# Kernel tuning notes

Measured on AMD Instinct MI355X. Metric: run time of the kernel, lower is better.

## Reference

```python
import jax, jax.numpy as jnp
import numpy as np

NUM_HEADS = 12
SPARSITY = 0.5

def setup_inputs() -> dict:
    key = jax.random.key(0)
    ks = jax.random.split(key, 5)
    B, N, C = 16, 577, 768
    x = jax.random.normal(ks[0], (B, N, C), dtype=jnp.float32)
    x_original = jax.random.normal(ks[1], (B, N, C), dtype=jnp.float32)
    qkv_w = jax.random.normal(ks[2], (3 * C, C), dtype=jnp.float32) * (C ** -0.5)
    proj_w = jax.random.normal(ks[3], (C, C), dtype=jnp.float32) * (C ** -0.5)
    proj_b = jax.random.normal(ks[4], (C,), dtype=jnp.float32) * 0.01
    return {"x": x, "x_original": x_original, "qkv_w": qkv_w,
            "proj_w": proj_w, "proj_b": proj_b, "num_prop": 57}

def reference(x, x_original, qkv_w, proj_w, proj_b, num_prop):
    B, N, C = x.shape
    H = NUM_HEADS
    hd = C // H
    scale = hd ** -0.5
    # qkv projection (no bias): [B,N,3C] -> q,k,v each [B,H,N,hd]
    qkv = (x @ qkv_w.T).reshape(B, N, 3, H, hd).transpose(2, 0, 3, 1, 4)
    q, k, v = qkv[0], qkv[1], qkv[2]
    attn = jax.nn.softmax(jnp.einsum('bhnd,bhmd->bhnm', q * scale, k), axis=-1)
    # sparsity threshold: keep entries >= the int(N*N*sparsity)-th largest per (b,h)
    if SPARSITY < 1:
        flat = attn.reshape(B, H, N * N)
        desc = -jnp.sort(-flat, axis=-1)  # descending
        sigma = desc[:, :, int(N * N * SPARSITY)][:, :, None, None]
        attn = jnp.where(attn >= sigma, attn, jnp.zeros((), attn.dtype))
    if num_prop > 0:
        K = N - num_prop  # tokens kept (incl. CLS)
        # token importance: max over heads of attention diagonal (excluding CLS)
        diag = jnp.diagonal(attn, axis1=-2, axis2=-1)[:, :, 1:]  # [B,H,N-1]
        token_rank = jnp.argsort(-diag.max(axis=1), axis=1)      # [B,N-1] desc
        index_kept = token_rank[:, :N - 1 - num_prop] + 1        # [B,K-1]
        index_kept = jnp.concatenate(
            [jnp.zeros((B, 1), index_kept.dtype), index_kept], axis=1)  # [B,K]
        # gather kept query rows of attn: [B,H,K,N]
        idx = jnp.broadcast_to(index_kept[:, None, :, None], (B, H, K, N))
        attn_kept = jnp.take_along_axis(attn, idx, axis=2)
        x_original = jnp.take_along_axis(
            x_original, jnp.broadcast_to(index_kept[:, :, None], (B, K, C)), axis=1)
        out = jnp.einsum('bhkn,bhnd->bhkd', attn_kept, v)
        out = out.transpose(0, 2, 1, 3).reshape(B, K, C)
    else:
        out = jnp.einsum('bhnm,bhmd->bhnd', attn, v)
        out = out.transpose(0, 2, 1, 3).reshape(B, N, C)
    out = out @ proj_w.T + proj_b
    return (out, x_original)
```

## Files before the change

### kernel.cpp

```cpp
#include <hip/hip_runtime.h>
#include <cstdint>
#include <cstddef>


namespace {
constexpr int B_  = 16;
constexpr int N_  = 577;
constexpr int C_  = 768;
constexpr int H_  = 12;
constexpr int HD_ = 64;
constexpr int BH_ = B_ * H_;
constexpr int KK_ = N_ - 57;
constexpr unsigned KIDX_ = 166464u;
constexpr int M1_ = B_ * N_;
constexpr int M2_ = B_ * KK_;
}

__device__ __forceinline__ void fma4(const float4& a, const float4& b, float& acc) {
  acc = __builtin_fmaf(a.x, b.x, acc);
  acc = __builtin_fmaf(a.y, b.y, acc);
  acc = __builtin_fmaf(a.z, b.z, acc);
  acc = __builtin_fmaf(a.w, b.w, acc);
}

__global__ __launch_bounds__(256) void qkv_gemm(
    const float* __restrict__ X, const float* __restrict__ W,
    float* __restrict__ qb, float* __restrict__ kb, float* __restrict__ vb) {
  __shared__ __align__(16) float Xs[64][68];
  __shared__ __align__(16) float Ws2[128][68];
  const int m0 = blockIdx.x * 64;
  const int n0 = blockIdx.y * 128;
  const int t = threadIdx.x;
  const int tx = t & 15, ty = t >> 4;
  float acc[4][8] = {};
  for (int k0 = 0; k0 < 768; k0 += 64) {
    __syncthreads();
    {
      const int c = t & 15, r0 = t >> 4;
#pragma unroll
      for (int s = 0; s < 4; s++) {
        int r = r0 + 16 * s;
        int gm = m0 + r;
        float4 v = make_float4(0.f, 0.f, 0.f, 0.f);
        if (gm < M1_) v = *(const float4*)&X[(size_t)gm * 768 + k0 + 4 * c];
        *(float4*)&Xs[r][4 * c] = v;
      }
#pragma unroll
      for (int s = 0; s < 8; s++) {
        int r = r0 + 16 * s;
        float4 v = *(const float4*)&W[(size_t)(n0 + r) * 768 + k0 + 4 * c];
        *(float4*)&Ws2[r][4 * c] = v;
      }
    }
    __syncthreads();
#pragma unroll 2
    for (int d4 = 0; d4 < 16; d4++) {
      float4 a4[4], b4[8];
#pragma unroll
      for (int i = 0; i < 4; i++) a4[i] = *(const float4*)&Xs[tx + 16 * i][4 * d4];
#pragma unroll
      for (int j = 0; j < 8; j++) b4[j] = *(const float4*)&Ws2[ty + 16 * j][4 * d4];
#pragma unroll
      for (int i = 0; i < 4; i++)
#pragma unroll
        for (int j = 0; j < 8; j++) fma4(a4[i], b4[j], acc[i][j]);
    }
  }
  for (int i = 0; i < 4; i++) {
    int gm = m0 + tx + 16 * i;
    if (gm >= M1_) continue;
    int b = gm / N_, n = gm % N_;
    for (int j = 0; j < 8; j++) {
      int gn = n0 + ty + 16 * j;
      int which = gn / C_, rem = gn % C_;
      int h = rem >> 6, d = rem & 63;
      float* dst = (which == 0) ? qb : (which == 1) ? kb : vb;
      dst[(((size_t)(b * H_ + h)) * N_ + n) * HD_ + d] = acc[i][j];
    }
  }
}

__global__ __launch_bounds__(256) void attn_stats(
    const float* __restrict__ qb, const float* __restrict__ kb,
    float* __restrict__ rowmax_g, float* __restrict__ rowsum_g,
    float* __restrict__ ldiag) {
  __shared__ __align__(16) float Qs[64][68];
  __shared__ __align__(16) float Ksf[128][68];
  const int bh = blockIdx.x;
  const int q0 = blockIdx.y * 64;
  const int t = threadIdx.x;
  const int tx = t & 15, ty = t >> 4;
  {
    const int c = t & 15, r0 = t >> 4;
#pragma unroll
    for (int s = 0; s < 4; s++) {
      int r = r0 + 16 * s;
      int gq = q0 + r;
      float4 v = make_float4(0.f, 0.f, 0.f, 0.f);
      if (gq < N_) v = *(const float4*)&qb[((size_t)bh * N_ + gq) * HD_ + 4 * c];
      v.x *= 0.125f; v.y *= 0.125f; v.z *= 0.125f; v.w *= 0.125f;
      *(float4*)&Qs[r][4 * c] = v;
    }
  }
  float m[4], ss[4];
#pragma unroll
  for (int i = 0; i < 4; i++) { m[i] = -INFINITY; ss[i] = 0.f; }
  for (int n0 = 0; n0 < N_; n0 += 128) {
    __syncthreads();
    {
      const int c = t & 15, r0 = t >> 4;
#pragma unroll
      for (int s = 0; s < 8; s++) {
        int r = r0 + 16 * s;
        int gn = n0 + r;
        float4 v = make_float4(0.f, 0.f, 0.f, 0.f);
        if (gn < N_) v = *(const float4*)&kb[((size_t)bh * N_ + gn) * HD_ + 4 * c];
        *(float4*)&Ksf[r][4 * c] = v;
      }
    }
    __syncthreads();
    float l[4][8];
#pragma unroll
    for (int i = 0; i < 4; i++)
#pragma unroll
      for (int j = 0; j < 8; j++) l[i][j] = 0.f;
#pragma unroll 2
    for (int d4 = 0; d4 < 16; d4++) {
      float4 a4[4], b4[8];
#pragma unroll
      for (int i = 0; i < 4; i++) a4[i] = *(const float4*)&Qs[tx + 16 * i][4 * d4];
#pragma unroll
      for (int j = 0; j < 8; j++) b4[j] = *(const float4*)&Ksf[ty + 16 * j][4 * d4];
#pragma unroll
      for (int i = 0; i < 4; i++)
#pragma unroll
        for (int j = 0; j < 8; j++) fma4(a4[i], b4[j], l[i][j]);
    }
#pragma unroll
    for (int i = 0; i < 4; i++) {
      int gq = q0 + tx + 16 * i;
      float tmax = -INFINITY;
#pragma unroll
      for (int j = 0; j < 8; j++)
        if (n0 + ty + 16 * j < N_) tmax = fmaxf(tmax, l[i][j]);
      float mn = fmaxf(m[i], tmax);
      ss[i] *= expf(m[i] - mn);
#pragma unroll
      for (int j = 0; j < 8; j++) {
        int col = n0 + ty + 16 * j;
        if (col < N_) {
          ss[i] += expf(l[i][j] - mn);
          if (col == gq) ldiag[(size_t)bh * N_ + gq] = l[i][j];
        }
      }
      m[i] = mn;
    }
  }
  __syncthreads();
  float* Mred = &Ksf[0][0];
  float* Sred = &Ksf[0][0] + 1024;
#pragma unroll
  for (int i = 0; i < 4; i++) {
    int row = tx + 16 * i;
    Mred[row * 16 + ty] = m[i];
    Sred[row * 16 + ty] = ss[i];
  }
  __syncthreads();
  if (t < 64) {
    int gq = q0 + t;
    if (gq < N_) {
      float M = -INFINITY;
      for (int k = 0; k < 16; k++) M = fmaxf(M, Mred[t * 16 + k]);
      float S = 0.f;
      for (int k = 0; k < 16; k++) S += expf(Mred[t * 16 + k] - M) * Sred[t * 16 + k];
      rowmax_g[(size_t)bh * N_ + gq] = M;
      rowsum_g[(size_t)bh * N_ + gq] = S;
    }
  }
}

template <int MODE>
__global__ __launch_bounds__(256) void hist_pass(
    const float* __restrict__ qb, const float* __restrict__ kb,
    const float* __restrict__ rowmax_g, const float* __restrict__ rowsum_g,
    const unsigned* __restrict__ pfx_in, unsigned* __restrict__ hist_out) {
  constexpr int HB = (MODE == 2) ? 256 : 4096;
  __shared__ __align__(16) float Qs[64][68];
  __shared__ __align__(16) float Ksf[128][68];
  __shared__ unsigned hloc[HB];
  const int bh = blockIdx.x;
  const int q0 = blockIdx.y * 64;
  const int t = threadIdx.x;
  const int tx = t & 15, ty = t >> 4;
  for (int i = t; i < HB; i += 256) hloc[i] = 0u;
  const unsigned pf = (MODE == 0) ? 0u : pfx_in[bh];
  {
    const int c = t & 15, r0 = t >> 4;
#pragma unroll
    for (int s = 0; s < 4; s++) {
      int r = r0 + 16 * s;
      int gq = q0 + r;
      float4 v = make_float4(0.f, 0.f, 0.f, 0.f);
      if (gq < N_) v = *(const float4*)&qb[((size_t)bh * N_ + gq) * HD_ + 4 * c];
      v.x *= 0.125f; v.y *= 0.125f; v.z *= 0.125f; v.w *= 0.125f;
      *(float4*)&Qs[r][4 * c] = v;
    }
  }
  float M[4], inv[4];
#pragma unroll
  for (int i = 0; i < 4; i++) {
    int gq = q0 + tx + 16 * i;
    if (gq < N_) {
      M[i] = rowmax_g[(size_t)bh * N_ + gq];
      inv[i] = 1.f / rowsum_g[(size_t)bh * N_ + gq];
    } else { M[i] = 0.f; inv[i] = 0.f; }
  }
  for (int n0 = 0; n0 < N_; n0 += 128) {
    __syncthreads();
    {
      const int c = t & 15, r0 = t >> 4;
#pragma unroll
      for (int s = 0; s < 8; s++) {
        int r = r0 + 16 * s;
        int gn = n0 + r;
        float4 v = make_float4(0.f, 0.f, 0.f, 0.f);
        if (gn < N_) v = *(const float4*)&kb[((size_t)bh * N_ + gn) * HD_ + 4 * c];
        *(float4*)&Ksf[r][4 * c] = v;
      }
    }
    __syncthreads();
    float l[4][8];
#pragma unroll
    for (int i = 0; i < 4; i++)
#pragma unroll
      for (int j = 0; j < 8; j++) l[i][j] = 0.f;
#pragma unroll 2
    for (int d4 = 0; d4 < 16; d4++) {
      float4 a4[4], b4[8];
#pragma unroll
      for (int i = 0; i < 4; i++) a4[i] = *(const float4*)&Qs[tx + 16 * i][4 * d4];
#pragma unroll
      for (int j = 0; j < 8; j++) b4[j] = *(const float4*)&Ksf[ty + 16 * j][4 * d4];
#pragma unroll
      for (int i = 0; i < 4; i++)
#pragma unroll
        for (int j = 0; j < 8; j++) fma4(a4[i], b4[j], l[i][j]);
    }
#pragma unroll
    for (int i = 0; i < 4; i++) {
      int gq = q0 + tx + 16 * i;
#pragma unroll
      for (int j = 0; j < 8; j++) {
        bool valid = (gq < N_) && (n0 + ty + 16 * j < N_);
        if (MODE == 0) {
          unsigned bin = 0xFFFFu;
          if (valid) {
            float e = expf(l[i][j] - M[i]);
            float v = e * inv[i];
            bin = __float_as_uint(v) >> 20;
          }
          unsigned lead = (unsigned)__builtin_amdgcn_readfirstlane((int)bin);
          unsigned long long mm = __ballot(bin == lead);
          if (bin == lead) {
            if (lead != 0xFFFFu && (t & 63) == (__ffsll((unsigned long long)mm) - 1))
              atomicAdd(&hloc[lead], (unsigned)__popcll(mm));
          } else if (bin != 0xFFFFu) {
            atomicAdd(&hloc[bin], 1u);
          }
        } else if (valid) {
          float e = expf(l[i][j] - M[i]);
          float v = e * inv[i];
          unsigned bits = __float_as_uint(v);
          if (MODE == 1) {
            if ((bits >> 20) == pf) atomicAdd(&hloc[(bits >> 8) & 0xFFFu], 1u);
          } else {
            if ((bits >> 8) == pf) atomicAdd(&hloc[bits & 0xFFu], 1u);
          }
        }
      }
    }
  }
  __syncthreads();
  for (int i = t; i < HB; i += 256)
    if (hloc[i]) atomicAdd(&hist_out[(size_t)bh * HB + i], hloc[i]);
}

__global__ __launch_bounds__(64) void select_level(
    const unsigned* __restrict__ hist, int nbins,
    const unsigned* __restrict__ krem_in, const unsigned* __restrict__ pfx_in,
    unsigned* __restrict__ krem_out, unsigned* __restrict__ pfx_out, int shift) {
  const int bh = blockIdx.x;
  const int l = threadIdx.x;
  const int seg = nbins / 64;
  const unsigned krem = krem_in ? krem_in[bh] : KIDX_;
  const unsigned* hb = hist + (size_t)bh * nbins;
  __shared__ unsigned ps[64];
  unsigned psum = 0;
  int hi = nbins - 1 - l * seg;
  for (int i = 0; i < seg; i++) psum += hb[hi - i];
  ps[l] = psum;
  __syncthreads();
  if (l == 0) {
    unsigned cum = 0, before = 0;
    int bin = 0;
    for (int j = 0; j < 64; j++) {
      if (cum + ps[j] > krem) {
        unsigned c = cum;
        int hj = nbins - 1 - j * seg;
        for (int i = 0; i < seg; i++) {
          unsigned cnt = hb[hj - i];
          if (c + cnt > krem) { bin = hj - i; before = c; break; }
          c += cnt;
        }
        break;
      }
      cum += ps[j];
    }
    unsigned p = pfx_in ? pfx_in[bh] : 0u;
    pfx_out[bh] = (p << shift) | (unsigned)bin;
    krem_out[bh] = krem - before;
  }
}

__global__ __launch_bounds__(576) void rank_kernel(
    const float* __restrict__ ldiag, const float* __restrict__ rowmax_g,
    const float* __restrict__ rowsum_g, const unsigned* __restrict__ sigbits,
    int* __restrict__ kept) {
  const int b = blockIdx.x;
  const int i = threadIdx.x;
  __shared__ float sc[576];
  float s = 0.f;
  for (int h = 0; h < H_; h++) {
    int bh = b * H_ + h;
    float l = ldiag[(size_t)bh * N_ + (i + 1)];
    float M = rowmax_g[(size_t)bh * N_ + (i + 1)];
    float inv = 1.f / rowsum_g[(size_t)bh * N_ + (i + 1)];
    float e = expf(l - M);
    float v = e * inv;
    float sg = __uint_as_float(sigbits[bh]);
    if (v >= sg) s = fmaxf(s, v);
  }
  sc[i] = s;
  __syncthreads();
  int r = 0;
  for (int j = 0; j < 576; j++) {
    float sj = sc[j];
    if (sj > s || (sj == s && j < i)) r++;
  }
  if (r < KK_ - 1) kept[b * KK_ + r + 1] = i + 1;
  if (i == 0) kept[b * KK_] = 0;
}

__global__ __launch_bounds__(256) void gather_x(
    const float* __restrict__ xo, const int* __restrict__ kept,
    float* __restrict__ out2) {
  const int bp = blockIdx.x;
  const int b = bp / KK_, p = bp % KK_;
  const int src = kept[b * KK_ + p];
  const float* s = xo + ((size_t)b * N_ + src) * C_;
  float* d = out2 + (size_t)bp * C_;
  for (int c = threadIdx.x; c < C_; c += 256) d[c] = s[c];
}

__global__ __launch_bounds__(256) void av_kernel(
    const float* __restrict__ qb, const float* __restrict__ kb,
    const float* __restrict__ vb, const int* __restrict__ kept,
    const float* __restrict__ rowmax_g, const float* __restrict__ rowsum_g,
    const unsigned* __restrict__ sigbits, float* __restrict__ out1) {
  __shared__ __align__(16) float Qs[64][68];
  __shared__ __align__(16) float Ksf[64][68];
  __shared__ __align__(16) float Vs[64][68];
  __shared__ int ridx[64];
  __shared__ float Ml[64], Il[64];
  const int bh = blockIdx.x;
  const int p0 = blockIdx.y * 64;
  const int b = bh / H_, h = bh % H_;
  const float sigma = __uint_as_float(sigbits[bh]);
  const int t = threadIdx.x;
  const int tx = t & 15, ty = t >> 4;
  if (t < 64) {
    int pp = p0 + t;
    int r = (pp < KK_) ? kept[b * KK_ + pp] : 0;
    ridx[t] = r;
    Ml[t] = rowmax_g[(size_t)bh * N_ + r];
    Il[t] = 1.f / rowsum_g[(size_t)bh * N_ + r];
  }
  __syncthreads();
  {
    const int c = t & 15, r0 = t >> 4;
#pragma unroll
    for (int s = 0; s < 4; s++) {
      int r = r0 + 16 * s;
      int gq = ridx[r];
      float4 v = *(const float4*)&qb[((size_t)bh * N_ + gq) * HD_ + 4 * c];
      v.x *= 0.125f; v.y *= 0.125f; v.z *= 0.125f; v.w *= 0.125f;
      *(float4*)&Qs[r][4 * c] = v;
    }
  }
  float M[4], inv[4];
#pragma unroll
  for (int i = 0; i < 4; i++) { int row = tx + 16 * i; M[i] = Ml[row]; inv[i] = Il[row]; }
  float acc[4][4] = {};
  for (int n0 = 0; n0 < N_; n0 += 64) {
    __syncthreads();
    {
      const int c = t & 15, r0 = t >> 4;
#pragma unroll
      for (int s = 0; s < 4; s++) {
        int r = r0 + 16 * s;
        int gn = n0 + r;
        float4 kv = make_float4(0.f, 0.f, 0.f, 0.f);
        float4 vv = make_float4(0.f, 0.f, 0.f, 0.f);
        if (gn < N_) {
          kv = *(const float4*)&kb[((size_t)bh * N_ + gn) * HD_ + 4 * c];
          vv = *(const float4*)&vb[((size_t)bh * N_ + gn) * HD_ + 4 * c];
        }
        *(float4*)&Ksf[r][4 * c] = kv;
        *(float4*)&Vs[r][4 * c] = vv;
      }
    }
    __syncthreads();
    float l[4][4];
#pragma unroll
    for (int i = 0; i < 4; i++)
#pragma unroll
      for (int j = 0; j < 4; j++) l[i][j] = 0.f;
#pragma unroll 4
    for (int d4 = 0; d4 < 16; d4++) {
      float4 a4[4], b4[4];
#pragma unroll
      for (int i = 0; i < 4; i++) a4[i] = *(const float4*)&Qs[tx + 16 * i][4 * d4];
#pragma unroll
      for (int j = 0; j < 4; j++) b4[j] = *(const float4*)&Ksf[4 * ty + j][4 * d4];
#pragma unroll
      for (int i = 0; i < 4; i++)
#pragma unroll
        for (int j = 0; j < 4; j++) fma4(a4[i], b4[j], l[i][j]);
    }
    __syncthreads();
#pragma unroll
    for (int i = 0; i < 4; i++) {
      float4 pv4;
      float* pp = (float*)&pv4;
#pragma unroll
      for (int j = 0; j < 4; j++) {
        float e = expf(l[i][j] - M[i]);
        float v = e * inv[i];
        pp[j] = (v >= sigma) ? v : 0.f;
      }
      *(float4*)&Ksf[tx + 16 * i][4 * ty] = pv4;
    }
    __syncthreads();
#pragma unroll 4
    for (int nb = 0; nb < 16; nb++) {
      float4 pa4[4];
#pragma unroll
      for (int i = 0; i < 4; i++) pa4[i] = *(const float4*)&Ksf[tx + 16 * i][4 * nb];
#pragma unroll
      for (int e = 0; e < 4; e++) {
        float4 vv4 = *(const float4*)&Vs[4 * nb + e][4 * ty];
        const float* pa = (const float*)&pa4[0];
#pragma unroll
        for (int i = 0; i < 4; i++) {
          float pvv = ((const float*)&pa4[i])[e];
          acc[i][0] = __builtin_fmaf(pvv, vv4.x, acc[i][0]);
          acc[i][1] = __builtin_fmaf(pvv, vv4.y, acc[i][1]);
          acc[i][2] = __builtin_fmaf(pvv, vv4.z, acc[i][2]);
          acc[i][3] = __builtin_fmaf(pvv, vv4.w, acc[i][3]);
        }
        (void)pa;
      }
    }
  }
#pragma unroll
  for (int i = 0; i < 4; i++) {
    int pp = p0 + tx + 16 * i;
    if (pp >= KK_) continue;
    float4 o = make_float4(acc[i][0], acc[i][1], acc[i][2], acc[i][3]);
    *(float4*)&out1[((size_t)(b * KK_ + pp)) * C_ + h * HD_ + 4 * ty] = o;
  }
}

__global__ __launch_bounds__(256) void proj_gemm(
    const float* __restrict__ Xi, const float* __restrict__ W,
    const float* __restrict__ bias, float* __restrict__ out) {
  __shared__ __align__(16) float Xs[64][68];
  __shared__ __align__(16) float Ws2[128][68];
  const int m0 = blockIdx.x * 64;
  const int n0 = blockIdx.y * 128;
  const int t = threadIdx.x;
  const int tx = t & 15, ty = t >> 4;
  float acc[4][8] = {};
  for (int k0 = 0; k0 < 768; k0 += 64) {
    __syncthreads();
    {
      const int c = t & 15, r0 = t >> 4;
#pragma unroll
      for (int s = 0; s < 4; s++) {
        int r = r0 + 16 * s;
        float4 v = *(const float4*)&Xi[(size_t)(m0 + r) * 768 + k0 + 4 * c];
        *(float4*)&Xs[r][4 * c] = v;
      }
#pragma unroll
      for (int s = 0; s < 8; s++) {
        int r = r0 + 16 * s;
        float4 v = *(const float4*)&W[(size_t)(n0 + r) * 768 + k0 + 4 * c];
        *(float4*)&Ws2[r][4 * c] = v;
      }
    }
    __syncthreads();
#pragma unroll 2
    for (int d4 = 0; d4 < 16; d4++) {
      float4 a4[4], b4[8];
#pragma unroll
      for (int i = 0; i < 4; i++) a4[i] = *(const float4*)&Xs[tx + 16 * i][4 * d4];
#pragma unroll
      for (int j = 0; j < 8; j++) b4[j] = *(const float4*)&Ws2[ty + 16 * j][4 * d4];
#pragma unroll
      for (int i = 0; i < 4; i++)
#pragma unroll
        for (int j = 0; j < 8; j++) fma4(a4[i], b4[j], acc[i][j]);
    }
  }
  for (int i = 0; i < 4; i++) {
    int gm = m0 + tx + 16 * i;
    for (int j = 0; j < 8; j++) {
      int gn = n0 + ty + 16 * j;
      out[(size_t)gm * C_ + gn] = acc[i][j] + bias[gn];
    }
  }
}

extern "C" void kernel_launch(void* const* d_in, const int* in_sizes, int n_in,
                              void* d_out, int out_size, void* d_ws, size_t ws_size,
                              hipStream_t stream) {
  (void)in_sizes; (void)n_in; (void)out_size; (void)ws_size;
  const float* x    = (const float*)d_in[0];
  const float* xo   = (const float*)d_in[1];
  const float* qkvw = (const float*)d_in[2];
  const float* pw   = (const float*)d_in[3];
  const float* pb   = (const float*)d_in[4];

  char* ws = (char*)d_ws;
  size_t off = 0;
  auto alloc = [&](size_t bytes) -> char* {
    char* p = ws + off;
    off += (bytes + 255) & ~(size_t)255;
    return p;
  };
  const size_t szQ    = (size_t)BH_ * N_ * HD_ * 4;
  const size_t szOut1 = (size_t)M2_ * C_ * 4;
  const size_t szRow  = (size_t)BH_ * N_ * 4;
  const size_t szH12  = (size_t)BH_ * 4096 * 4;
  const size_t szH3   = (size_t)BH_ * 256 * 4;

  float* qb     = (float*)alloc(szQ);
  float* kb     = (float*)alloc(szQ);
  float* vb     = (float*)alloc(szQ);
  float* out1   = (float*)alloc(szOut1);
  float* ldiag  = (float*)alloc(szRow);
  float* rowmax = (float*)alloc(szRow);
  float* rowsum = (float*)alloc(szRow);
  unsigned* hist1 = (unsigned*)alloc(szH12);
  unsigned* hist2 = (unsigned*)alloc(szH12);
  unsigned* hist3 = (unsigned*)alloc(szH3);
  unsigned* pfx1  = (unsigned*)alloc(BH_ * 4);
  unsigned* krem1 = (unsigned*)alloc(BH_ * 4);
  unsigned* pfx2  = (unsigned*)alloc(BH_ * 4);
  unsigned* krem2 = (unsigned*)alloc(BH_ * 4);
  unsigned* pfx3  = (unsigned*)alloc(BH_ * 4);
  unsigned* krem3 = (unsigned*)alloc(BH_ * 4);
  int* kept       = (int*)alloc((size_t)B_ * KK_ * 4);

  hipMemsetAsync(hist1, 0, szH12, stream);
  hipMemsetAsync(hist2, 0, szH12, stream);
  hipMemsetAsync(hist3, 0, szH3, stream);

  qkv_gemm<<<dim3(145, 18), 256, 0, stream>>>(x, qkvw, qb, kb, vb);
  attn_stats<<<dim3(BH_, 10), 256, 0, stream>>>(qb, kb, rowmax, rowsum, ldiag);
  hist_pass<0><<<dim3(BH_, 10), 256, 0, stream>>>(qb, kb, rowmax, rowsum, nullptr, hist1);
  select_level<<<BH_, 64, 0, stream>>>(hist1, 4096, nullptr, nullptr, krem1, pfx1, 12);
  hist_pass<1><<<dim3(BH_, 10), 256, 0, stream>>>(qb, kb, rowmax, rowsum, pfx1, hist2);
  select_level<<<BH_, 64, 0, stream>>>(hist2, 4096, krem1, pfx1, krem2, pfx2, 12);
  hist_pass<2><<<dim3(BH_, 10), 256, 0, stream>>>(qb, kb, rowmax, rowsum, pfx2, hist3);
  select_level<<<BH_, 64, 0, stream>>>(hist3, 256, krem2, pfx2, krem3, pfx3, 8);
  rank_kernel<<<B_, 576, 0, stream>>>(ldiag, rowmax, rowsum, pfx3, kept);

  float* outp = (float*)d_out;
  gather_x<<<M2_, 256, 0, stream>>>(xo, kept, outp + (size_t)M2_ * C_);
  av_kernel<<<dim3(BH_, 9), 256, 0, stream>>>(qb, kb, vb, kept, rowmax, rowsum, pfx3, out1);
  proj_gemm<<<dim3(130, 6), 256, 0, stream>>>(out1, pw, pb, outp);
}
```

Before: 1.801 ms.

## Fuse attention stats with first histogram pass and enlarge GEMM tiles

Merges the row max/sum statistics kernel and the first radix-histogram pass into one kernel. It holds all 5 column tiles of logits in registers, so the QK^T product is computed once instead of twice. The QKV and output projection GEMMs move from 64x128 to 128x128 tiles with a 32-wide k step, giving each thread an 8x8 accumulator. Both changes raise register pressure: the 160 logits per thread in the fused kernel may spill or cut occupancy, and the bigger GEMM tiles launch fewer blocks.

```diff
diff --git a/kernel.cpp b/kernel.cpp
--- a/kernel.cpp
+++ b/kernel.cpp
@@ -14,6 +14,7 @@
 constexpr unsigned KIDX_ = 166464u;
 constexpr int M1_ = B_ * N_;
 constexpr int M2_ = B_ * KK_;
+constexpr int NT_ = 5;
 }
 
 __device__ __forceinline__ void fma4(const float4& a, const float4& b, float& acc) {
@@ -26,47 +27,43 @@
 __global__ __launch_bounds__(256) void qkv_gemm(
     const float* __restrict__ X, const float* __restrict__ W,
     float* __restrict__ qb, float* __restrict__ kb, float* __restrict__ vb) {
-  __shared__ __align__(16) float Xs[64][68];
-  __shared__ __align__(16) float Ws2[128][68];
-  const int m0 = blockIdx.x * 64;
+  __shared__ __align__(16) float Xs[128][36];
+  __shared__ __align__(16) float Ws2[128][36];
+  const int m0 = blockIdx.x * 128;
   const int n0 = blockIdx.y * 128;
   const int t = threadIdx.x;
   const int tx = t & 15, ty = t >> 4;
-  float acc[4][8] = {};
-  for (int k0 = 0; k0 < 768; k0 += 64) {
+  float acc[8][8] = {};
+  for (int k0 = 0; k0 < 768; k0 += 32) {
     __syncthreads();
     {
-      const int c = t & 15, r0 = t >> 4;
+      const int c = t & 7, r0 = t >> 3;
 #pragma unroll
       for (int s = 0; s < 4; s++) {
-        int r = r0 + 16 * s;
+        int r = r0 + 32 * s;
         int gm = m0 + r;
         float4 v = make_float4(0.f, 0.f, 0.f, 0.f);
         if (gm < M1_) v = *(const float4*)&X[(size_t)gm * 768 + k0 + 4 * c];
         *(float4*)&Xs[r][4 * c] = v;
-      }
-#pragma unroll
-      for (int s = 0; s < 8; s++) {
-        int r = r0 + 16 * s;
-        float4 v = *(const float4*)&W[(size_t)(n0 + r) * 768 + k0 + 4 * c];
-        *(float4*)&Ws2[r][4 * c] = v;
-      }
-    }
-    __syncthreads();
-#pragma unroll 2
-    for (int d4 = 0; d4 < 16; d4++) {
-      float4 a4[4], b4[8];
-#pragma unroll
-      for (int i = 0; i < 4; i++) a4[i] = *(const float4*)&Xs[tx + 16 * i][4 * d4];
+        float4 w = *(const float4*)&W[(size_t)(n0 + r) * 768 + k0 + 4 * c];
+        *(float4*)&Ws2[r][4 * c] = w;
+      }
+    }
+    __syncthreads();
+#pragma unroll
+    for (int d4 = 0; d4 < 8; d4++) {
+      float4 a4[8], b4[8];
+#pragma unroll
+      for (int i = 0; i < 8; i++) a4[i] = *(const float4*)&Xs[tx + 16 * i][4 * d4];
 #pragma unroll
       for (int j = 0; j < 8; j++) b4[j] = *(const float4*)&Ws2[ty + 16 * j][4 * d4];
 #pragma unroll
-      for (int i = 0; i < 4; i++)
+      for (int i = 0; i < 8; i++)
 #pragma unroll
         for (int j = 0; j < 8; j++) fma4(a4[i], b4[j], acc[i][j]);
     }
   }
-  for (int i = 0; i < 4; i++) {
+  for (int i = 0; i < 8; i++) {
     int gm = m0 + tx + 16 * i;
     if (gm >= M1_) continue;
     int b = gm / N_, n = gm % N_;
@@ -80,16 +77,19 @@
   }
 }
 
-__global__ __launch_bounds__(256) void attn_stats(
+__global__ __launch_bounds__(256) void stats_hist1(
     const float* __restrict__ qb, const float* __restrict__ kb,
     float* __restrict__ rowmax_g, float* __restrict__ rowsum_g,
-    float* __restrict__ ldiag) {
+    float* __restrict__ ldiag, unsigned* __restrict__ hist1) {
   __shared__ __align__(16) float Qs[64][68];
   __shared__ __align__(16) float Ksf[128][68];
+  __shared__ unsigned hloc[4096];
+  __shared__ float Mrow[64], Srow[64];
   const int bh = blockIdx.x;
   const int q0 = blockIdx.y * 64;
   const int t = threadIdx.x;
   const int tx = t & 15, ty = t >> 4;
+  for (int i = t; i < 4096; i += 256) hloc[i] = 0u;
   {
     const int c = t & 15, r0 = t >> 4;
 #pragma unroll
@@ -102,10 +102,17 @@
       *(float4*)&Qs[r][4 * c] = v;
     }
   }
-  float m[4], ss[4];
-#pragma unroll
-  for (int i = 0; i < 4; i++) { m[i] = -INFINITY; ss[i] = 0.f; }
-  for (int n0 = 0; n0 < N_; n0 += 128) {
+  float l[NT_][4][8];
+#pragma unroll
+  for (int tt = 0; tt < NT_; tt++)
+#pragma unroll
+    for (int i = 0; i < 4; i++)
+#pragma unroll
+      for (int j = 0; j < 8; j++) l[tt][i][j] = 0.f;
+
+#pragma unroll
+  for (int tt = 0; tt < NT_; tt++) {
+    const int n0 = tt * 128;
     __syncthreads();
     {
       const int c = t & 15, r0 = t >> 4;
@@ -119,11 +126,6 @@
       }
     }
     __syncthreads();
-    float l[4][8];
-#pragma unroll
-    for (int i = 0; i < 4; i++)
-#pragma unroll
-      for (int j = 0; j < 8; j++) l[i][j] = 0.f;
 #pragma unroll 2
     for (int d4 = 0; d4 < 16; d4++) {
       float4 a4[4], b4[8];
@@ -134,49 +136,88 @@
 #pragma unroll
       for (int i = 0; i < 4; i++)
 #pragma unroll
-        for (int j = 0; j < 8; j++) fma4(a4[i], b4[j], l[i][j]);
-    }
+        for (int j = 0; j < 8; j++) fma4(a4[i], b4[j], l[tt][i][j]);
+    }
+  }
+  __syncthreads();
+  float* Mred = &Ksf[0][0];
+  float* Sred = &Ksf[0][0] + 1024;
+#pragma unroll
+  for (int i = 0; i < 4; i++) {
+    float mx = -INFINITY;
+#pragma unroll
+    for (int tt = 0; tt < NT_; tt++)
+#pragma unroll
+      for (int j = 0; j < 8; j++) {
+        int col = tt * 128 + ty + 16 * j;
+        if (col < N_) mx = fmaxf(mx, l[tt][i][j]);
+      }
+    Mred[(tx + 16 * i) * 16 + ty] = mx;
+  }
+  __syncthreads();
+  if (t < 64) {
+    float M = -INFINITY;
+    for (int k = 0; k < 16; k++) M = fmaxf(M, Mred[t * 16 + k]);
+    Mrow[t] = M;
+    if (q0 + t < N_) rowmax_g[(size_t)bh * N_ + q0 + t] = M;
+  }
+  __syncthreads();
+  float Mi_[4];
+#pragma unroll
+  for (int i = 0; i < 4; i++) Mi_[i] = Mrow[tx + 16 * i];
+#pragma unroll
+  for (int i = 0; i < 4; i++) {
+    float s = 0.f;
+#pragma unroll
+    for (int tt = 0; tt < NT_; tt++)
+#pragma unroll
+      for (int j = 0; j < 8; j++) {
+        int col = tt * 128 + ty + 16 * j;
+        if (col < N_) s += expf(l[tt][i][j] - Mi_[i]);
+      }
+    Sred[(tx + 16 * i) * 16 + ty] = s;
+  }
+  __syncthreads();
+  if (t < 64) {
+    float S = 0.f;
+    for (int k = 0; k < 16; k++) S += Sred[t * 16 + k];
+    Srow[t] = S;
+    if (q0 + t < N_) rowsum_g[(size_t)bh * N_ + q0 + t] = S;
+  }
+  __syncthreads();
+  float inv[4];
+#pragma unroll
+  for (int i = 0; i < 4; i++) inv[i] = 1.f / Srow[tx + 16 * i];
+#pragma unroll
+  for (int tt = 0; tt < NT_; tt++) {
 #pragma unroll
     for (int i = 0; i < 4; i++) {
       int gq = q0 + tx + 16 * i;
-      float tmax = -INFINITY;
-#pragma unroll
-      for (int j = 0; j < 8; j++)
-        if (n0 + ty + 16 * j < N_) tmax = fmaxf(tmax, l[i][j]);
-      float mn = fmaxf(m[i], tmax);
-      ss[i] *= expf(m[i] - mn);
 #pragma unroll
       for (int j = 0; j < 8; j++) {
-        int col = n0 + ty + 16 * j;
-        if (col < N_) {
-          ss[i] += expf(l[i][j] - mn);
-          if (col == gq) ldiag[(size_t)bh * N_ + gq] = l[i][j];
+        int col = tt * 128 + ty + 16 * j;
+        bool valid = (gq < N_) && (col < N_);
+        unsigned bin = 0xFFFFu;
+        if (valid) {
+          float e = expf(l[tt][i][j] - Mi_[i]);
+          float v = e * inv[i];
+          bin = __float_as_uint(v) >> 20;
+          if (col == gq) ldiag[(size_t)bh * N_ + gq] = l[tt][i][j];
         }
-      }
-      m[i] = mn;
-    }
-  }
-  __syncthreads();
-  float* Mred = &Ksf[0][0];
-  float* Sred = &Ksf[0][0] + 1024;
-#pragma unroll
-  for (int i = 0; i < 4; i++) {
-    int row = tx + 16 * i;
-    Mred[row * 16 + ty] = m[i];
-    Sred[row * 16 + ty] = ss[i];
-  }
-  __syncthreads();
-  if (t < 64) {
-    int gq = q0 + t;
-    if (gq < N_) {
-      float M = -INFINITY;
-      for (int k = 0; k < 16; k++) M = fmaxf(M, Mred[t * 16 + k]);
-      float S = 0.f;
-      for (int k = 0; k < 16; k++) S += expf(Mred[t * 16 + k] - M) * Sred[t * 16 + k];
-      rowmax_g[(size_t)bh * N_ + gq] = M;
-      rowsum_g[(size_t)bh * N_ + gq] = S;
-    }
-  }
+        unsigned lead = (unsigned)__builtin_amdgcn_readfirstlane((int)bin);
+        unsigned long long mm = __ballot(bin == lead);
+        if (bin == lead) {
+          if (lead != 0xFFFFu && (t & 63) == (__ffsll((unsigned long long)mm) - 1))
+            atomicAdd(&hloc[lead], (unsigned)__popcll(mm));
+        } else if (bin != 0xFFFFu) {
+          atomicAdd(&hloc[bin], 1u);
+        }
+      }
+    }
+  }
+  __syncthreads();
+  for (int i = t; i < 4096; i += 256)
+    if (hloc[i]) atomicAdd(&hist1[(size_t)bh * 4096 + i], hloc[i]);
 }
 
 template <int MODE>
@@ -193,7 +234,7 @@
   const int t = threadIdx.x;
   const int tx = t & 15, ty = t >> 4;
   for (int i = t; i < HB; i += 256) hloc[i] = 0u;
-  const unsigned pf = (MODE == 0) ? 0u : pfx_in[bh];
+  const unsigned pf = pfx_in[bh];
   {
     const int c = t & 15, r0 = t >> 4;
 #pragma unroll
@@ -251,23 +292,7 @@
       int gq = q0 + tx + 16 * i;
 #pragma unroll
       for (int j = 0; j < 8; j++) {
-        bool valid = (gq < N_) && (n0 + ty + 16 * j < N_);
-        if (MODE == 0) {
-          unsigned bin = 0xFFFFu;
-          if (valid) {
-            float e = expf(l[i][j] - M[i]);
-            float v = e * inv[i];
-            bin = __float_as_uint(v) >> 20;
-          }
-          unsigned lead = (unsigned)__builtin_amdgcn_readfirstlane((int)bin);
-          unsigned long long mm = __ballot(bin == lead);
-          if (bin == lead) {
-            if (lead != 0xFFFFu && (t & 63) == (__ffsll((unsigned long long)mm) - 1))
-              atomicAdd(&hloc[lead], (unsigned)__popcll(mm));
-          } else if (bin != 0xFFFFu) {
-            atomicAdd(&hloc[bin], 1u);
-          }
-        } else if (valid) {
+        if ((gq < N_) && (n0 + ty + 16 * j < N_)) {
           float e = expf(l[i][j] - M[i]);
           float v = e * inv[i];
           unsigned bits = __float_as_uint(v);
@@ -459,7 +484,6 @@
 #pragma unroll
       for (int e = 0; e < 4; e++) {
         float4 vv4 = *(const float4*)&Vs[4 * nb + e][4 * ty];
-        const float* pa = (const float*)&pa4[0];
 #pragma unroll
         for (int i = 0; i < 4; i++) {
           float pvv = ((const float*)&pa4[i])[e];
@@ -468,7 +492,6 @@
           acc[i][2] = __builtin_fmaf(pvv, vv4.z, acc[i][2]);
           acc[i][3] = __builtin_fmaf(pvv, vv4.w, acc[i][3]);
         }
-        (void)pa;
       }
     }
   }
@@ -484,45 +507,41 @@
 __global__ __launch_bounds__(256) void proj_gemm(
     const float* __restrict__ Xi, const float* __restrict__ W,
     const float* __restrict__ bias, float* __restrict__ out) {
-  __shared__ __align__(16) float Xs[64][68];
-  __shared__ __align__(16) float Ws2[128][68];
-  const int m0 = blockIdx.x * 64;
+  __shared__ __align__(16) float Xs[128][36];
+  __shared__ __align__(16) float Ws2[128][36];
+  const int m0 = blockIdx.x * 128;
   const int n0 = blockIdx.y * 128;
   const int t = threadIdx.x;
   const int tx = t & 15, ty = t >> 4;
-  float acc[4][8] = {};
-  for (int k0 = 0; k0 < 768; k0 += 64) {
+  float acc[8][8] = {};
+  for (int k0 = 0; k0 < 768; k0 += 32) {
     __syncthreads();
     {
-      const int c = t & 15, r0 = t >> 4;
+      const int c = t & 7, r0 = t >> 3;
 #pragma unroll
       for (int s = 0; s < 4; s++) {
-        int r = r0 + 16 * s;
+        int r = r0 + 32 * s;
         float4 v = *(const float4*)&Xi[(size_t)(m0 + r) * 768 + k0 + 4 * c];
         *(float4*)&Xs[r][4 * c] = v;
-      }
-#pragma unroll
-      for (int s = 0; s < 8; s++) {
-        int r = r0 + 16 * s;
-        float4 v = *(const float4*)&W[(size_t)(n0 + r) * 768 + k0 + 4 * c];
-        *(float4*)&Ws2[r][4 * c] = v;
-      }
-    }
-    __syncthreads();
-#pragma unroll 2
-    for (int d4 = 0; d4 < 16; d4++) {
-      float4 a4[4], b4[8];
-#pragma unroll
-      for (int i = 0; i < 4; i++) a4[i] = *(const float4*)&Xs[tx + 16 * i][4 * d4];
+        float4 w = *(const float4*)&W[(size_t)(n0 + r) * 768 + k0 + 4 * c];
+        *(float4*)&Ws2[r][4 * c] = w;
+      }
+    }
+    __syncthreads();
+#pragma unroll
+    for (int d4 = 0; d4 < 8; d4++) {
+      float4 a4[8], b4[8];
+#pragma unroll
+      for (int i = 0; i < 8; i++) a4[i] = *(const float4*)&Xs[tx + 16 * i][4 * d4];
 #pragma unroll
       for (int j = 0; j < 8; j++) b4[j] = *(const float4*)&Ws2[ty + 16 * j][4 * d4];
 #pragma unroll
-      for (int i = 0; i < 4; i++)
+      for (int i = 0; i < 8; i++)
 #pragma unroll
         for (int j = 0; j < 8; j++) fma4(a4[i], b4[j], acc[i][j]);
     }
   }
-  for (int i = 0; i < 4; i++) {
+  for (int i = 0; i < 8; i++) {
     int gm = m0 + tx + 16 * i;
     for (int j = 0; j < 8; j++) {
       int gn = n0 + ty + 16 * j;
@@ -568,7 +587,7 @@
   unsigned* krem1 = (unsigned*)alloc(BH_ * 4);
   unsigned* pfx2  = (unsigned*)alloc(BH_ * 4);
   unsigned* krem2 = (unsigned*)alloc(BH_ * 4);
-  unsigned* pfx3  = (unsigned*)alloc(BH_ * 4);
+  unsigned* sigb  = (unsigned*)alloc(BH_ * 4);
   unsigned* krem3 = (unsigned*)alloc(BH_ * 4);
   int* kept       = (int*)alloc((size_t)B_ * KK_ * 4);
 
@@ -576,18 +595,17 @@
   hipMemsetAsync(hist2, 0, szH12, stream);
   hipMemsetAsync(hist3, 0, szH3, stream);
 
-  qkv_gemm<<<dim3(145, 18), 256, 0, stream>>>(x, qkvw, qb, kb, vb);
-  attn_stats<<<dim3(BH_, 10), 256, 0, stream>>>(qb, kb, rowmax, rowsum, ldiag);
-  hist_pass<0><<<dim3(BH_, 10), 256, 0, stream>>>(qb, kb, rowmax, rowsum, nullptr, hist1);
+  qkv_gemm<<<dim3(73, 18), 256, 0, stream>>>(x, qkvw, qb, kb, vb);
+  stats_hist1<<<dim3(BH_, 10), 256, 0, stream>>>(qb, kb, rowmax, rowsum, ldiag, hist1);
   select_level<<<BH_, 64, 0, stream>>>(hist1, 4096, nullptr, nullptr, krem1, pfx1, 12);
   hist_pass<1><<<dim3(BH_, 10), 256, 0, stream>>>(qb, kb, rowmax, rowsum, pfx1, hist2);
   select_level<<<BH_, 64, 0, stream>>>(hist2, 4096, krem1, pfx1, krem2, pfx2, 12);
   hist_pass<2><<<dim3(BH_, 10), 256, 0, stream>>>(qb, kb, rowmax, rowsum, pfx2, hist3);
-  select_level<<<BH_, 64, 0, stream>>>(hist3, 256, krem2, pfx2, krem3, pfx3, 8);
-  rank_kernel<<<B_, 576, 0, stream>>>(ldiag, rowmax, rowsum, pfx3, kept);
+  select_level<<<BH_, 64, 0, stream>>>(hist3, 256, krem2, pfx2, krem3, sigb, 8);
+  rank_kernel<<<B_, 576, 0, stream>>>(ldiag, rowmax, rowsum, sigb, kept);
 
   float* outp = (float*)d_out;
   gather_x<<<M2_, 256, 0, stream>>>(xo, kept, outp + (size_t)M2_ * C_);
-  av_kernel<<<dim3(BH_, 9), 256, 0, stream>>>(qb, kb, vb, kept, rowmax, rowsum, pfx3, out1);
-  proj_gemm<<<dim3(130, 6), 256, 0, stream>>>(out1, pw, pb, outp);
-}
+  av_kernel<<<dim3(BH_, 9), 256, 0, stream>>>(qb, kb, vb, kept, rowmax, rowsum, sigb, out1);
+  proj_gemm<<<dim3(65, 6), 256, 0, stream>>>(out1, pw, pb, outp);
+}
```

Result: slower. 2.189 ms (+21.5%).
